# Optimization experiments

Measured on AMD Instinct MI355X. Metric: run time of the kernel, lower is better.

The kernel has to match this reference:

```python
import jax, jax.numpy as jnp
import numpy as np
from jax import lax

B, T, F, K = 128, 1024, 128, 32


def setup_inputs() -> dict:
    key = jax.random.key(0)
    k1, k2, k3 = jax.random.split(key, 3)
    inp = jax.random.normal(k1, (B, T, F), dtype=jnp.float32)
    mask = jnp.ones((B, T), dtype=bool)
    W_emit = jax.random.normal(k2, (F, K), dtype=jnp.float32) * 0.02
    transition = jax.random.normal(k3, (K, K), dtype=jnp.float32) * 0.1
    return {"input": inp, "mask": mask, "W_emit": W_emit, "transition": transition}


def reference(input, mask, W_emit, transition):
    # emissions: [B, T, K]
    emission = jnp.einsum('btf,fk->btk', input, W_emit)
    alpha0 = emission[:, 0]                      # [B, K]
    em_seq = jnp.swapaxes(emission[:, 1:], 0, 1)  # [T-1, B, K]
    mk_seq = jnp.swapaxes(mask[:, 1:], 0, 1)      # [T-1, B]

    def step(alpha, xs):
        em_t, m_t = xs
        # alpha_t[b,j] = logsumexp_i(alpha[b,i] + transition[i,j]) + em_t[b,j]
        new = jax.scipy.special.logsumexp(alpha[:, :, None] + transition[None], axis=1) + em_t
        alpha = jnp.where(m_t[:, None], new, alpha)
        return alpha, None

    alpha, _ = lax.scan(step, alpha0, (em_seq, mk_seq))
    log_z = jax.scipy.special.logsumexp(alpha, axis=-1)  # [B]
    return jnp.sum(log_z)
```

## Files before the change

kernel.cpp:

```cpp
#include <hip/hip_runtime.h>
#include <hip/hip_bf16.h>

#define Bb 128
#define Tt 1024
#define Ff 128
#define Kk 32
#define KS 36
#define KE 36
#define LOG32 3.4657359027997265f

typedef __attribute__((ext_vector_type(8))) short bf16x8;
typedef __attribute__((ext_vector_type(4))) float f32x4;

__device__ __forceinline__ float bf2f(unsigned u) {
    return __uint_as_float(u << 16);
}
__device__ __forceinline__ unsigned short f2bf(float f) {
    unsigned u = __float_as_uint(f);
    u = (u + 0x7fffu + ((u >> 16) & 1u)) >> 16;
    return (unsigned short)u;
}
__device__ __forceinline__ unsigned bfpk2(float a, float b) {
    __hip_bfloat162 h = __float22bfloat162_rn(make_float2(a, b));
    unsigned u;
    __builtin_memcpy(&u, &h, sizeof(u));
    return u;
}

__global__ __launch_bounds__(128, 4) void chunk_kernel(
    const float* __restrict__ inp, const int* __restrict__ mask,
    const float* __restrict__ W, const float* __restrict__ trans,
    unsigned short* __restrict__ SQ, float* __restrict__ out)
{
    __shared__ __align__(16) float gl[32 * KE];
    __shared__ __align__(16) unsigned short Sl[2][32 * KS];
    const int tid = threadIdx.x;
    const int w = tid >> 6, lane = tid & 63;
    const int q = lane >> 4, n = lane & 15;
    const int b = blockIdx.x >> 5, c = blockIdx.x & 31;
    const int tw = c * 32 + w * 16;

    if (blockIdx.x == 0 && tid == 0) out[0] = 0.f;

    const int* mbp = mask + (long)b * Tt;
    int mybit = (lane < 16) ? (mbp[tw + lane] != 0) : 0;
    unsigned mbits = (unsigned)__ballot(mybit) & 0xffffu;
    if (c == 0 && w == 0) mbits &= ~1u;

    bf16x8 A0, A1;
    #pragma unroll
    for (int j = 0; j < 8; ++j) {
        A0[j] = (short)f2bf(__expf(trans[(q * 8 + j) * Kk + n]));
        A1[j] = (short)f2bf(__expf(trans[(q * 8 + j) * Kk + 16 + n]));
    }

    const f32x4 zz = {0.f, 0.f, 0.f, 0.f};
    f32x4 E0 = zz, E1 = zz;
    const float* xrow = inp + ((long)b * Tt + tw) * Ff;
    #pragma unroll
    for (int kt = 0; kt < 4; ++kt) {
        const int f0 = kt * 32 + q * 8;
        float4 a0v = *(const float4*)&xrow[n * Ff + f0];
        float4 a1v = *(const float4*)&xrow[n * Ff + f0 + 4];
        uint4 ua = make_uint4(bfpk2(a0v.x, a0v.y), bfpk2(a0v.z, a0v.w),
                              bfpk2(a1v.x, a1v.y), bfpk2(a1v.z, a1v.w));
        bf16x8 Aw = __builtin_bit_cast(bf16x8, ua);
        float wl[8], wh[8];
        #pragma unroll
        for (int jj = 0; jj < 8; ++jj) {
            wl[jj] = W[(f0 + jj) * Kk + n];
            wh[jj] = W[(f0 + jj) * Kk + 16 + n];
        }
        uint4 uc = make_uint4(bfpk2(wl[0], wl[1]), bfpk2(wl[2], wl[3]),
                              bfpk2(wl[4], wl[5]), bfpk2(wl[6], wl[7]));
        uint4 ud = make_uint4(bfpk2(wh[0], wh[1]), bfpk2(wh[2], wh[3]),
                              bfpk2(wh[4], wh[5]), bfpk2(wh[6], wh[7]));
        bf16x8 Blo = __builtin_bit_cast(bf16x8, uc);
        bf16x8 Bhi = __builtin_bit_cast(bf16x8, ud);
        E0 = __builtin_amdgcn_mfma_f32_16x16x32_bf16(Aw, Blo, E0, 0, 0, 0);
        E1 = __builtin_amdgcn_mfma_f32_16x16x32_bf16(Aw, Bhi, E1, 0, 0, 0);
    }
    #pragma unroll
    for (int r = 0; r < 4; ++r) {
        gl[(w * 16 + q * 4 + r) * KE + n]      = __expf(E0[r] - LOG32);
        gl[(w * 16 + q * 4 + r) * KE + 16 + n] = __expf(E1[r] - LOG32);
    }

    unsigned short* Sw = Sl[w];
    for (int i = lane; i < (32 * KS) / 2; i += 64)
        ((unsigned*)Sw)[i] = 0u;
    if (lane < 32) Sw[lane * KS + lane] = 0x3f80;

    #pragma unroll
    for (int ls = 0; ls < 16; ++ls) {
        if (!((mbits >> ls) & 1u)) continue;
        uint2 xa = *(const uint2*)&Sw[ n       * KS + q * 8];
        uint2 xb = *(const uint2*)&Sw[ n       * KS + q * 8 + 4];
        uint2 ya = *(const uint2*)&Sw[(n + 16) * KS + q * 8];
        uint2 yb = *(const uint2*)&Sw[(n + 16) * KS + q * 8 + 4];
        uint4 u0 = make_uint4(xa.x, xa.y, xb.x, xb.y);
        uint4 u1 = make_uint4(ya.x, ya.y, yb.x, yb.y);
        bf16x8 B0 = __builtin_bit_cast(bf16x8, u0);
        bf16x8 B1 = __builtin_bit_cast(bf16x8, u1);
        f32x4 D00 = __builtin_amdgcn_mfma_f32_16x16x32_bf16(A0, B0, zz, 0, 0, 0);
        f32x4 D01 = __builtin_amdgcn_mfma_f32_16x16x32_bf16(A0, B1, zz, 0, 0, 0);
        f32x4 D10 = __builtin_amdgcn_mfma_f32_16x16x32_bf16(A1, B0, zz, 0, 0, 0);
        f32x4 D11 = __builtin_amdgcn_mfma_f32_16x16x32_bf16(A1, B1, zz, 0, 0, 0);
        float4 g0 = *(const float4*)&gl[(w * 16 + ls) * KE + q * 4];
        float4 g1 = *(const float4*)&gl[(w * 16 + ls) * KE + 16 + q * 4];
        *(uint2*)&Sw[ n       * KS      + q * 4] =
            make_uint2(bfpk2(D00[0] * g0.x, D00[1] * g0.y), bfpk2(D00[2] * g0.z, D00[3] * g0.w));
        *(uint2*)&Sw[(n + 16) * KS      + q * 4] =
            make_uint2(bfpk2(D01[0] * g0.x, D01[1] * g0.y), bfpk2(D01[2] * g0.z, D01[3] * g0.w));
        *(uint2*)&Sw[ n       * KS + 16 + q * 4] =
            make_uint2(bfpk2(D10[0] * g1.x, D10[1] * g1.y), bfpk2(D10[2] * g1.z, D10[3] * g1.w));
        *(uint2*)&Sw[(n + 16) * KS + 16 + q * 4] =
            make_uint2(bfpk2(D11[0] * g1.x, D11[1] * g1.y), bfpk2(D11[2] * g1.z, D11[3] * g1.w));
    }

    __syncthreads();

    const unsigned short* SlA = Sl[0];
    const unsigned short* SlB = Sl[1];
    bf16x8 Af;
    #pragma unroll
    for (int j = 0; j < 8; ++j)
        Af[j] = (short)SlB[(q * 8 + j) * KS + w * 16 + n];
    uint2 xa = *(const uint2*)&SlA[ n       * KS + q * 8];
    uint2 xb = *(const uint2*)&SlA[ n       * KS + q * 8 + 4];
    uint2 ya = *(const uint2*)&SlA[(n + 16) * KS + q * 8];
    uint2 yb = *(const uint2*)&SlA[(n + 16) * KS + q * 8 + 4];
    uint4 u0 = make_uint4(xa.x, xa.y, xb.x, xb.y);
    uint4 u1 = make_uint4(ya.x, ya.y, yb.x, yb.y);
    bf16x8 B0 = __builtin_bit_cast(bf16x8, u0);
    bf16x8 B1 = __builtin_bit_cast(bf16x8, u1);
    f32x4 D0 = __builtin_amdgcn_mfma_f32_16x16x32_bf16(Af, B0, zz, 0, 0, 0);
    f32x4 D1 = __builtin_amdgcn_mfma_f32_16x16x32_bf16(Af, B1, zz, 0, 0, 0);

    unsigned short* sq = SQ + (long)(b * 32 + c) * 1024;
    #pragma unroll
    for (int r = 0; r < 4; ++r) {
        sq[(w * 16 + q * 4 + r) * 32 + n]      = f2bf(D0[r]);
        sq[(w * 16 + q * 4 + r) * 32 + 16 + n] = f2bf(D1[r]);
    }
}

__global__ __launch_bounds__(64) void apply_kernel(
    const float* __restrict__ inp, const int* __restrict__ mask,
    const float* __restrict__ W, const unsigned short* __restrict__ SQ,
    float* __restrict__ out)
{
    const int b = blockIdx.x, lane = threadIdx.x & 63, k = lane & 31;
    const int* mbp = mask + (long)b * Tt;

    const unsigned short* sqb = SQ + (long)b * 32 * 1024;
    uint4 cur[4], nxt[4];
    #pragma unroll
    for (int e = 0; e < 4; ++e) cur[e] = *(const uint4*)(sqb + k * 32 + 8 * e);
    #pragma unroll
    for (int e = 0; e < 4; ++e) nxt[e] = *(const uint4*)(sqb + 1024 + k * 32 + 8 * e);

    int cnt = 0;
    #pragma unroll
    for (int it = 0; it < 16; ++it) cnt += (mbp[it * 64 + lane] != 0) ? 1 : 0;
    #pragma unroll
    for (int off = 32; off; off >>= 1) cnt += __shfl_xor(cnt, off);
    cnt -= (mbp[0] != 0) ? 1 : 0;

    const float* x0 = inp + (long)b * Tt * Ff;
    float a0 = 0.f;
    #pragma unroll 4
    for (int f = 0; f < Ff; ++f)
        a0 = fmaf(x0[f], W[f * Kk + k], a0);

    float c0 = __int_as_float(__builtin_amdgcn_readlane(__float_as_int(a0), 0));
    float p = __expf(a0 - c0);
    float csum = c0 + (float)cnt * LOG32;

    #pragma unroll 2
    for (int c = 0; c < 32; ++c) {
        uint4 pf[4];
        if (c + 2 < 32) {
            const unsigned short* s2 = sqb + (c + 2) * 1024 + k * 32;
            #pragma unroll
            for (int e = 0; e < 4; ++e) pf[e] = *(const uint4*)(s2 + 8 * e);
        }
        const int pi = __float_as_int(p);
        float q0 = 0.f, q1 = 0.f, q2 = 0.f, q3 = 0.f;
        #define RL(j) __int_as_float(__builtin_amdgcn_readlane(pi, (j)))
        #define ACC2(word, j, acc) \
            acc = fmaf(bf2f((word) & 0xffffu), RL(j), acc); \
            acc = fmaf(bf2f((word) >> 16),     RL((j) + 1), acc);
        ACC2(cur[0].x,  0, q0) ACC2(cur[0].y,  2, q0) ACC2(cur[0].z,  4, q0) ACC2(cur[0].w,  6, q0)
        ACC2(cur[1].x,  8, q1) ACC2(cur[1].y, 10, q1) ACC2(cur[1].z, 12, q1) ACC2(cur[1].w, 14, q1)
        ACC2(cur[2].x, 16, q2) ACC2(cur[2].y, 18, q2) ACC2(cur[2].z, 20, q2) ACC2(cur[2].w, 22, q2)
        ACC2(cur[3].x, 24, q3) ACC2(cur[3].y, 26, q3) ACC2(cur[3].z, 28, q3) ACC2(cur[3].w, 30, q3)
        #undef ACC2
        #undef RL
        float qq = (q0 + q1) + (q2 + q3);
        if (c == 15) {
            float s0 = __int_as_float(__builtin_amdgcn_readlane(__float_as_int(qq), 0));
            csum += __logf(s0);
            qq *= (1.0f / s0);
        }
        p = qq;
        #pragma unroll
        for (int e = 0; e < 4; ++e) { cur[e] = nxt[e]; nxt[e] = pf[e]; }
    }

    float sum = p;
    #pragma unroll
    for (int off = 16; off > 0; off >>= 1)
        sum += __shfl_xor(sum, off);
    if (lane == 0)
        atomicAdd(out, csum + __logf(sum));
}

extern "C" void kernel_launch(void* const* d_in, const int* in_sizes, int n_in,
                              void* d_out, int out_size, void* d_ws, size_t ws_size,
                              hipStream_t stream)
{
    const float* inp   = (const float*)d_in[0];
    const int*   mask  = (const int*)d_in[1];
    const float* W     = (const float*)d_in[2];
    const float* trans = (const float*)d_in[3];
    float* out = (float*)d_out;
    unsigned short* SQ = (unsigned short*)d_ws;

    chunk_kernel<<<dim3(Bb * 32), dim3(128), 0, stream>>>(inp, mask, W, trans, SQ, out);
    apply_kernel<<<dim3(Bb), dim3(64), 0, stream>>>(inp, mask, W, SQ, out);
}
```

Measured before the change: 129.1 us.

## Keep chunk transfer matrix in registers using 32x32 MFMA and permlane swaps

```diff
diff --git a/kernel.cpp b/kernel.cpp
--- a/kernel.cpp
+++ b/kernel.cpp
@@ -5,20 +5,15 @@
 #define Tt 1024
 #define Ff 128
 #define Kk 32
-#define KS 36
 #define KE 36
 #define LOG32 3.4657359027997265f
 
 typedef __attribute__((ext_vector_type(8))) short bf16x8;
 typedef __attribute__((ext_vector_type(4))) float f32x4;
+typedef __attribute__((ext_vector_type(16))) float f32x16;
 
 __device__ __forceinline__ float bf2f(unsigned u) {
     return __uint_as_float(u << 16);
-}
-__device__ __forceinline__ unsigned short f2bf(float f) {
-    unsigned u = __float_as_uint(f);
-    u = (u + 0x7fffu + ((u >> 16) & 1u)) >> 16;
-    return (unsigned short)u;
 }
 __device__ __forceinline__ unsigned bfpk2(float a, float b) {
     __hip_bfloat162 h = __float22bfloat162_rn(make_float2(a, b));
@@ -26,45 +21,32 @@
     __builtin_memcpy(&u, &h, sizeof(u));
     return u;
 }
-
-__global__ __launch_bounds__(128, 4) void chunk_kernel(
+__device__ __forceinline__ void plswap(unsigned &a, unsigned &b) {
+    asm("v_permlane32_swap_b32 %0, %1" : "+v"(a), "+v"(b));
+}
+
+__global__ __launch_bounds__(64, 4) void chunk_kernel(
     const float* __restrict__ inp, const int* __restrict__ mask,
     const float* __restrict__ W, const float* __restrict__ trans,
     unsigned short* __restrict__ SQ, float* __restrict__ out)
 {
     __shared__ __align__(16) float gl[32 * KE];
-    __shared__ __align__(16) unsigned short Sl[2][32 * KS];
-    const int tid = threadIdx.x;
-    const int w = tid >> 6, lane = tid & 63;
-    const int q = lane >> 4, n = lane & 15;
+    const int lane = threadIdx.x & 63;
+    const int q = (lane >> 4) & 3, n = lane & 15;
+    const int c32 = lane & 31, hi = lane >> 5;
     const int b = blockIdx.x >> 5, c = blockIdx.x & 31;
-    const int tw = c * 32 + w * 16;
-
-    if (blockIdx.x == 0 && tid == 0) out[0] = 0.f;
+    const int t0 = c * 32;
+
+    if (blockIdx.x == 0 && lane == 0) out[0] = 0.f;
 
     const int* mbp = mask + (long)b * Tt;
-    int mybit = (lane < 16) ? (mbp[tw + lane] != 0) : 0;
-    unsigned mbits = (unsigned)__ballot(mybit) & 0xffffu;
-    if (c == 0 && w == 0) mbits &= ~1u;
-
-    bf16x8 A0, A1;
-    #pragma unroll
-    for (int j = 0; j < 8; ++j) {
-        A0[j] = (short)f2bf(__expf(trans[(q * 8 + j) * Kk + n]));
-        A1[j] = (short)f2bf(__expf(trans[(q * 8 + j) * Kk + 16 + n]));
-    }
-
-    const f32x4 zz = {0.f, 0.f, 0.f, 0.f};
-    f32x4 E0 = zz, E1 = zz;
-    const float* xrow = inp + ((long)b * Tt + tw) * Ff;
+    unsigned mbits = (unsigned)__ballot(mbp[t0 + c32] != 0);
+    if (c == 0) mbits &= ~1u;
+
+    bf16x8 Wlo[4], Whi[4];
     #pragma unroll
     for (int kt = 0; kt < 4; ++kt) {
         const int f0 = kt * 32 + q * 8;
-        float4 a0v = *(const float4*)&xrow[n * Ff + f0];
-        float4 a1v = *(const float4*)&xrow[n * Ff + f0 + 4];
-        uint4 ua = make_uint4(bfpk2(a0v.x, a0v.y), bfpk2(a0v.z, a0v.w),
-                              bfpk2(a1v.x, a1v.y), bfpk2(a1v.z, a1v.w));
-        bf16x8 Aw = __builtin_bit_cast(bf16x8, ua);
         float wl[8], wh[8];
         #pragma unroll
         for (int jj = 0; jj < 8; ++jj) {
@@ -75,73 +57,84 @@
                               bfpk2(wl[4], wl[5]), bfpk2(wl[6], wl[7]));
         uint4 ud = make_uint4(bfpk2(wh[0], wh[1]), bfpk2(wh[2], wh[3]),
                               bfpk2(wh[4], wh[5]), bfpk2(wh[6], wh[7]));
-        bf16x8 Blo = __builtin_bit_cast(bf16x8, uc);
-        bf16x8 Bhi = __builtin_bit_cast(bf16x8, ud);
-        E0 = __builtin_amdgcn_mfma_f32_16x16x32_bf16(Aw, Blo, E0, 0, 0, 0);
-        E1 = __builtin_amdgcn_mfma_f32_16x16x32_bf16(Aw, Bhi, E1, 0, 0, 0);
-    }
-    #pragma unroll
-    for (int r = 0; r < 4; ++r) {
-        gl[(w * 16 + q * 4 + r) * KE + n]      = __expf(E0[r] - LOG32);
-        gl[(w * 16 + q * 4 + r) * KE + 16 + n] = __expf(E1[r] - LOG32);
-    }
-
-    unsigned short* Sw = Sl[w];
-    for (int i = lane; i < (32 * KS) / 2; i += 64)
-        ((unsigned*)Sw)[i] = 0u;
-    if (lane < 32) Sw[lane * KS + lane] = 0x3f80;
-
-    #pragma unroll
-    for (int ls = 0; ls < 16; ++ls) {
+        Wlo[kt] = __builtin_bit_cast(bf16x8, uc);
+        Whi[kt] = __builtin_bit_cast(bf16x8, ud);
+    }
+
+    const f32x4 zz = {0.f, 0.f, 0.f, 0.f};
+    #pragma unroll
+    for (int s = 0; s < 2; ++s) {
+        f32x4 E0 = zz, E1 = zz;
+        const float* xrow = inp + ((long)b * Tt + t0 + s * 16) * Ff;
+        #pragma unroll
+        for (int kt = 0; kt < 4; ++kt) {
+            const int f0 = kt * 32 + q * 8;
+            float4 a0v = *(const float4*)&xrow[n * Ff + f0];
+            float4 a1v = *(const float4*)&xrow[n * Ff + f0 + 4];
+            uint4 ua = make_uint4(bfpk2(a0v.x, a0v.y), bfpk2(a0v.z, a0v.w),
+                                  bfpk2(a1v.x, a1v.y), bfpk2(a1v.z, a1v.w));
+            bf16x8 Aw = __builtin_bit_cast(bf16x8, ua);
+            E0 = __builtin_amdgcn_mfma_f32_16x16x32_bf16(Aw, Wlo[kt], E0, 0, 0, 0);
+            E1 = __builtin_amdgcn_mfma_f32_16x16x32_bf16(Aw, Whi[kt], E1, 0, 0, 0);
+        }
+        #pragma unroll
+        for (int r = 0; r < 4; ++r) {
+            gl[(s * 16 + q * 4 + r) * KE + n]      = __expf(E0[r] - LOG32);
+            gl[(s * 16 + q * 4 + r) * KE + 16 + n] = __expf(E1[r] - LOG32);
+        }
+    }
+
+    float Elo[8], Ehi[8];
+    #pragma unroll
+    for (int j = 0; j < 8; ++j) {
+        Elo[j] = __expf(trans[(8 * hi + j) * Kk + c32]);
+        Ehi[j] = __expf(trans[(16 + 8 * hi + j) * Kk + c32]);
+    }
+
+    unsigned B1[4], B2[4];
+    #pragma unroll
+    for (int w2 = 0; w2 < 4; ++w2) {
+        const int r0 = 8 * hi + 2 * w2;
+        B1[w2] = (r0 == c32 ? 0x3f80u : 0u) | (r0 + 1 == c32 ? (0x3f80u << 16) : 0u);
+        const int r2 = 16 + r0;
+        B2[w2] = (r2 == c32 ? 0x3f80u : 0u) | (r2 + 1 == c32 ? (0x3f80u << 16) : 0u);
+    }
+
+    #pragma unroll
+    for (int ls = 0; ls < 32; ++ls) {
         if (!((mbits >> ls) & 1u)) continue;
-        uint2 xa = *(const uint2*)&Sw[ n       * KS + q * 8];
-        uint2 xb = *(const uint2*)&Sw[ n       * KS + q * 8 + 4];
-        uint2 ya = *(const uint2*)&Sw[(n + 16) * KS + q * 8];
-        uint2 yb = *(const uint2*)&Sw[(n + 16) * KS + q * 8 + 4];
-        uint4 u0 = make_uint4(xa.x, xa.y, xb.x, xb.y);
-        uint4 u1 = make_uint4(ya.x, ya.y, yb.x, yb.y);
-        bf16x8 B0 = __builtin_bit_cast(bf16x8, u0);
-        bf16x8 B1 = __builtin_bit_cast(bf16x8, u1);
-        f32x4 D00 = __builtin_amdgcn_mfma_f32_16x16x32_bf16(A0, B0, zz, 0, 0, 0);
-        f32x4 D01 = __builtin_amdgcn_mfma_f32_16x16x32_bf16(A0, B1, zz, 0, 0, 0);
-        f32x4 D10 = __builtin_amdgcn_mfma_f32_16x16x32_bf16(A1, B0, zz, 0, 0, 0);
-        f32x4 D11 = __builtin_amdgcn_mfma_f32_16x16x32_bf16(A1, B1, zz, 0, 0, 0);
-        float4 g0 = *(const float4*)&gl[(w * 16 + ls) * KE + q * 4];
-        float4 g1 = *(const float4*)&gl[(w * 16 + ls) * KE + 16 + q * 4];
-        *(uint2*)&Sw[ n       * KS      + q * 4] =
-            make_uint2(bfpk2(D00[0] * g0.x, D00[1] * g0.y), bfpk2(D00[2] * g0.z, D00[3] * g0.w));
-        *(uint2*)&Sw[(n + 16) * KS      + q * 4] =
-            make_uint2(bfpk2(D01[0] * g0.x, D01[1] * g0.y), bfpk2(D01[2] * g0.z, D01[3] * g0.w));
-        *(uint2*)&Sw[ n       * KS + 16 + q * 4] =
-            make_uint2(bfpk2(D10[0] * g1.x, D10[1] * g1.y), bfpk2(D10[2] * g1.z, D10[3] * g1.w));
-        *(uint2*)&Sw[(n + 16) * KS + 16 + q * 4] =
-            make_uint2(bfpk2(D11[0] * g1.x, D11[1] * g1.y), bfpk2(D11[2] * g1.z, D11[3] * g1.w));
-    }
-
-    __syncthreads();
-
-    const unsigned short* SlA = Sl[0];
-    const unsigned short* SlB = Sl[1];
-    bf16x8 Af;
-    #pragma unroll
-    for (int j = 0; j < 8; ++j)
-        Af[j] = (short)SlB[(q * 8 + j) * KS + w * 16 + n];
-    uint2 xa = *(const uint2*)&SlA[ n       * KS + q * 8];
-    uint2 xb = *(const uint2*)&SlA[ n       * KS + q * 8 + 4];
-    uint2 ya = *(const uint2*)&SlA[(n + 16) * KS + q * 8];
-    uint2 yb = *(const uint2*)&SlA[(n + 16) * KS + q * 8 + 4];
-    uint4 u0 = make_uint4(xa.x, xa.y, xb.x, xb.y);
-    uint4 u1 = make_uint4(ya.x, ya.y, yb.x, yb.y);
-    bf16x8 B0 = __builtin_bit_cast(bf16x8, u0);
-    bf16x8 B1 = __builtin_bit_cast(bf16x8, u1);
-    f32x4 D0 = __builtin_amdgcn_mfma_f32_16x16x32_bf16(Af, B0, zz, 0, 0, 0);
-    f32x4 D1 = __builtin_amdgcn_mfma_f32_16x16x32_bf16(Af, B1, zz, 0, 0, 0);
+        const float g = gl[ls * KE + c32];
+        uint4 fa = make_uint4(bfpk2(g * Elo[0], g * Elo[1]), bfpk2(g * Elo[2], g * Elo[3]),
+                              bfpk2(g * Elo[4], g * Elo[5]), bfpk2(g * Elo[6], g * Elo[7]));
+        uint4 fb = make_uint4(bfpk2(g * Ehi[0], g * Ehi[1]), bfpk2(g * Ehi[2], g * Ehi[3]),
+                              bfpk2(g * Ehi[4], g * Ehi[5]), bfpk2(g * Ehi[6], g * Ehi[7]));
+        bf16x8 Alo = __builtin_bit_cast(bf16x8, fa);
+        bf16x8 Ahi = __builtin_bit_cast(bf16x8, fb);
+        uint4 ub1 = make_uint4(B1[0], B1[1], B1[2], B1[3]);
+        uint4 ub2 = make_uint4(B2[0], B2[1], B2[2], B2[3]);
+        f32x16 Cc = {0.f, 0.f, 0.f, 0.f, 0.f, 0.f, 0.f, 0.f,
+                     0.f, 0.f, 0.f, 0.f, 0.f, 0.f, 0.f, 0.f};
+        Cc = __builtin_amdgcn_mfma_f32_32x32x16_bf16(Alo, __builtin_bit_cast(bf16x8, ub1), Cc, 0, 0, 0);
+        Cc = __builtin_amdgcn_mfma_f32_32x32x16_bf16(Ahi, __builtin_bit_cast(bf16x8, ub2), Cc, 0, 0, 0);
+        unsigned wa = bfpk2(Cc[0], Cc[1]),   wb = bfpk2(Cc[2], Cc[3]);
+        unsigned xa = bfpk2(Cc[4], Cc[5]),   xb = bfpk2(Cc[6], Cc[7]);
+        unsigned ya = bfpk2(Cc[8], Cc[9]),   yb = bfpk2(Cc[10], Cc[11]);
+        unsigned za = bfpk2(Cc[12], Cc[13]), zb = bfpk2(Cc[14], Cc[15]);
+        plswap(wa, xa); B1[0] = wa; B1[2] = xa;
+        plswap(wb, xb); B1[1] = wb; B1[3] = xb;
+        plswap(ya, za); B2[0] = ya; B2[2] = za;
+        plswap(yb, zb); B2[1] = yb; B2[3] = zb;
+    }
 
     unsigned short* sq = SQ + (long)(b * 32 + c) * 1024;
     #pragma unroll
-    for (int r = 0; r < 4; ++r) {
-        sq[(w * 16 + q * 4 + r) * 32 + n]      = f2bf(D0[r]);
-        sq[(w * 16 + q * 4 + r) * 32 + 16 + n] = f2bf(D1[r]);
+    for (int w2 = 0; w2 < 4; ++w2) {
+        const int r0 = 8 * hi + 2 * w2;
+        sq[ r0      * 32 + c32] = (unsigned short)(B1[w2] & 0xffffu);
+        sq[(r0 + 1) * 32 + c32] = (unsigned short)(B1[w2] >> 16);
+        const int r2 = 16 + r0;
+        sq[ r2      * 32 + c32] = (unsigned short)(B2[w2] & 0xffffu);
+        sq[(r2 + 1) * 32 + c32] = (unsigned short)(B2[w2] >> 16);
     }
 }
 
@@ -227,6 +220,6 @@
     float* out = (float*)d_out;
     unsigned short* SQ = (unsigned short*)d_ws;
 
-    chunk_kernel<<<dim3(Bb * 32), dim3(128), 0, stream>>>(inp, mask, W, trans, SQ, out);
+    chunk_kernel<<<dim3(Bb * 32), dim3(64), 0, stream>>>(inp, mask, W, trans, SQ, out);
     apply_kernel<<<dim3(Bb), dim3(64), 0, stream>>>(inp, mask, W, SQ, out);
 }
```

New measurement: 135.5 us. 5.0% more time.
